# Kernel optimization log

Hardware: AMD Instinct MI355X
Metric: run time of the kernel (lower is better)

Reference implementation:

```python
import jax, jax.numpy as jnp
import numpy as np

N = 50000      # nodes
E = 800000     # edges
DIN = 256
DH = 256
DOUT = 64


def setup_inputs() -> dict:
    key = jax.random.key(0)
    ks = jax.random.split(key, 8)
    x = jax.random.normal(ks[0], (N, DIN), dtype=jnp.float32)
    edge_index = jax.random.randint(ks[1], (2, E), 0, N, dtype=jnp.int64)
    s = 0.05
    W1 = jax.random.normal(ks[2], (DIN, DH), dtype=jnp.float32) * s
    b1 = jnp.zeros((DH,), dtype=jnp.float32)
    W2 = jax.random.normal(ks[3], (DH, DH), dtype=jnp.float32) * s
    b2 = jnp.zeros((DH,), dtype=jnp.float32)
    W3 = jax.random.normal(ks[4], (DH, DOUT), dtype=jnp.float32) * s
    b3 = jnp.zeros((DOUT,), dtype=jnp.float32)
    return {"x": x, "edge_index": edge_index, "W1": W1, "b1": b1,
            "W2": W2, "b2": b2, "W3": W3, "b3": b3}


def gcn_conv(x, src, dst, deg_inv_sqrt, W, b):
    # x: [N, din] -> [N, dout]. PyG GCNConv: h = D^{-1/2}(A+I)D^{-1/2} (x W) + b
    n = x.shape[0]
    h = x @ W                                   # [N, dout]
    norm = deg_inv_sqrt[src] * deg_inv_sqrt[dst]  # [E+N]
    msgs = h[src] * norm[:, None]               # gather + scale, [E+N, dout]
    out = jax.ops.segment_sum(msgs, dst, num_segments=n)  # scatter-add
    return out + b


def _loops(edge_index, n):
    # add self loops, compute symmetric normalization degrees
    sl = jnp.arange(n, dtype=edge_index.dtype)
    src = jnp.concatenate([edge_index[0], sl])
    dst = jnp.concatenate([edge_index[1], sl])
    deg = jax.ops.segment_sum(jnp.ones_like(dst, dtype=jnp.float32), dst, num_segments=n)
    dis = jnp.where(deg > 0, jax.lax.rsqrt(deg), 0.0)
    return src, dst, dis


def reference(x, edge_index, W1, b1, W2, b2, W3, b3):
    src, dst, dis = _loops(edge_index, x.shape[0])
    h = jax.nn.relu(gcn_conv(x, src, dst, dis, W1, b1))   # dropout: eval no-op
    h = jax.nn.relu(gcn_conv(h, src, dst, dis, W2, b2))
    out = gcn_conv(h, src, dst, dis, W3, b3)              # batch=None -> no pooling
    return out
```

## Files before the change

kernel.cpp:

```cpp
#include <hip/hip_runtime.h>
#include <hip/hip_fp8.h>
#include <cstdint>
#include <cstddef>

typedef unsigned short u16;
typedef _Float16 f16x8 __attribute__((ext_vector_type(8)));
typedef float f32x2 __attribute__((ext_vector_type(2)));
typedef float f32x4 __attribute__((ext_vector_type(4)));

#if defined(__has_builtin)
#if __has_builtin(__builtin_amdgcn_cvt_pk_f32_fp8) && __has_builtin(__builtin_amdgcn_cvt_pk_fp8_f32)
#define FP8_BUILTIN 1
#endif
#endif

__device__ __forceinline__ float h2f(u16 u) {
  return (float)__builtin_bit_cast(_Float16, u);
}
__device__ __forceinline__ u16 f2h(float f) {
  return __builtin_bit_cast(u16, (_Float16)f);
}
__device__ __forceinline__ unsigned char ftofp8(float f) {
#ifdef FP8_BUILTIN
  return (unsigned char)(__builtin_amdgcn_cvt_pk_fp8_f32(f, f, 0, false) & 0xFF);
#else
  return __hip_fp8_e4m3(f).__x;
#endif
}

__device__ __forceinline__ void async16(u16* lds, const u16* g) {
  __builtin_amdgcn_global_load_lds(
      (const __attribute__((address_space(1))) unsigned int*)g,
      (__attribute__((address_space(3))) unsigned int*)lds, 16, 0, 0);
}

__device__ __forceinline__ void fma8p(float* a, float d, uint2 p) {
#ifdef FP8_BUILTIN
  f32x2 v0 = __builtin_amdgcn_cvt_pk_f32_fp8((int)p.x, false);
  f32x2 v1 = __builtin_amdgcn_cvt_pk_f32_fp8((int)p.x, true);
  f32x2 v2 = __builtin_amdgcn_cvt_pk_f32_fp8((int)p.y, false);
  f32x2 v3 = __builtin_amdgcn_cvt_pk_f32_fp8((int)p.y, true);
  a[0] += d * v0.x; a[1] += d * v0.y; a[2] += d * v1.x; a[3] += d * v1.y;
  a[4] += d * v2.x; a[5] += d * v2.y; a[6] += d * v3.x; a[7] += d * v3.y;
#else
  const unsigned char* b = (const unsigned char*)&p;
#pragma unroll
  for (int k = 0; k < 8; ++k) {
    __hip_fp8_e4m3 v; v.__x = b[k];
    a[k] += d * (float)v;
  }
#endif
}

__device__ __forceinline__ f16x8 cvt8(const float* p) {
  float4 a = *(const float4*)p;
  float4 b = *(const float4*)(p + 4);
  f16x8 r;
  r[0] = (_Float16)a.x; r[1] = (_Float16)a.y; r[2] = (_Float16)a.z; r[3] = (_Float16)a.w;
  r[4] = (_Float16)b.x; r[5] = (_Float16)b.y; r[6] = (_Float16)b.z; r[7] = (_Float16)b.w;
  return r;
}

__device__ __forceinline__ int wave_is64(const void* ep) {
  const unsigned* p = (const unsigned*)ep;
  const int lane = threadIdx.x & 63;
  unsigned v = p[2 * lane + 1] | p[2 * (lane + 64) + 1];
  unsigned long long bal = __ballot(v != 0u);
  return (bal == 0ull) ? 1 : 0;
}

__device__ __forceinline__ int edge_at(const void* ep, int is64, long long idx) {
  if (is64) return (int)((const long long*)ep)[idx];
  return ((const int*)ep)[idx];
}

#define NCHUNK 64

__global__ void zero_f32(float* p, int n) {
  int i = blockIdx.x * 256 + threadIdx.x;
  if (i < n) p[i] = 0.f;
}

__global__ __launch_bounds__(256) void prep_all(
    const float* __restrict__ W1, u16* __restrict__ wt1,
    const float* __restrict__ W2, u16* __restrict__ wt2,
    const float* __restrict__ W3, u16* __restrict__ wt3,
    const void* __restrict__ ep, int* __restrict__ cnt,
    int E, int N, int DIN, int DH, int DOUT,
    int nb_w1, int nb_w2, int nb_w3) {
  int b = blockIdx.x;
  if (b < nb_w1) {
    int idx = b * 256 + threadIdx.x;
    if (idx < DIN * DH) {
      int n = idx / DIN, k = idx % DIN;
      wt1[idx] = f2h(W1[k * DH + n]);
    }
    return;
  }
  b -= nb_w1;
  if (b < nb_w2) {
    int idx = b * 256 + threadIdx.x;
    if (idx < DH * DH) {
      int n = idx / DH, k = idx % DH;
      wt2[idx] = f2h(W2[k * DH + n]);
    }
    return;
  }
  b -= nb_w2;
  if (b < nb_w3) {
    int idx = b * 256 + threadIdx.x;
    if (idx < DH * DOUT) {
      int n = idx / DH, k = idx % DH;
      wt3[idx] = f2h(W3[k * DOUT + n]);
    }
    return;
  }
  b -= nb_w3;
  {
    __shared__ int h[256];
    h[threadIdx.x] = 0;
    __syncthreads();
    int is64 = wave_is64(ep);
    const int per = (E + NCHUNK - 1) / NCHUNK;
    const int e0 = b * per, e1 = min(e0 + per, E);
    for (int e = e0 + (int)threadIdx.x; e < e1; e += 256) {
      int d = edge_at(ep, is64, (long long)E + e);
      d = min(max(d, 0), N - 1);
      atomicAdd(&h[d >> 8], 1);
    }
    __syncthreads();
    cnt[threadIdx.x * NCHUNK + b] = h[threadIdx.x];
  }
}

__device__ __forceinline__ void bases_in_lds(const int* __restrict__ cnt,
                                             int nbuck, int E, int* bl, int* ws4) {
  const int t = threadIdx.x, lane = t & 63, w = t >> 6;
  int tot = 0;
  if (t < nbuck)
#pragma unroll 8
    for (int c = 0; c < NCHUNK; ++c) tot += cnt[t * NCHUNK + c];
  int inc = tot;
#pragma unroll
  for (int o = 1; o < 64; o <<= 1) {
    int u = __shfl_up(inc, o, 64);
    if (lane >= o) inc += u;
  }
  if (lane == 63) ws4[w] = inc;
  __syncthreads();
  if (t == 0) {
    int run = 0;
#pragma unroll
    for (int k = 0; k < 4; ++k) { int v = ws4[k]; ws4[k + 4] = run; run += v; }
  }
  __syncthreads();
  bl[t] = ws4[w + 4] + inc - tot;
  if (t == 0) bl[nbuck] = E;
  __syncthreads();
}

__global__ __launch_bounds__(256) void csr_bucket(const void* __restrict__ ep,
                                                  const int* __restrict__ cnt,
                                                  unsigned* __restrict__ tmp,
                                                  int E, int N, int nbuck) {
  __shared__ int bl[257];
  __shared__ int cur[256];
  __shared__ int ws4[8];
  const int chunk = blockIdx.x;
  const int t = threadIdx.x;
  bases_in_lds(cnt, nbuck, E, bl, ws4);
  if (t < nbuck) {
    int partial = 0;
    for (int c = 0; c < chunk; ++c) partial += cnt[t * NCHUNK + c];
    cur[t] = bl[t] + partial;
  }
  __syncthreads();
  int is64 = wave_is64(ep);
  const int per = (E + NCHUNK - 1) / NCHUNK;
  const int e0 = chunk * per, e1 = min(e0 + per, E);
  for (int e = e0 + t; e < e1; e += 256) {
    int s = edge_at(ep, is64, e);
    int d = edge_at(ep, is64, (long long)E + e);
    s = min(max(s, 0), N - 1);
    d = min(max(d, 0), N - 1);
    int pos = atomicAdd(&cur[d >> 8], 1);
    tmp[pos] = ((unsigned)d << 16) | (unsigned)s;
  }
}

__global__ __launch_bounds__(256) void csr_final(const unsigned* __restrict__ tmp,
                                                 const int* __restrict__ cnt,
                                                 int* __restrict__ rp,
                                                 float* __restrict__ dis,
                                                 u16* __restrict__ col,
                                                 int N, int E, int nbuck) {
  __shared__ int bl[257];
  __shared__ int hcnt[256];
  __shared__ int curs[256];
  __shared__ int ws4[8];
  const int b = blockIdx.x;
  const int node0 = b * 256;
  const int t = threadIdx.x, lane = t & 63, w = t >> 6;
  bases_in_lds(cnt, nbuck, E, bl, ws4);
  const int k0 = bl[b], k1 = bl[b + 1];
  hcnt[t] = 0;
  __syncthreads();
  for (int k = k0 + t; k < k1; k += 256)
    atomicAdd(&hcnt[(int)(tmp[k] >> 16) - node0], 1);
  __syncthreads();
  const int v = hcnt[t];
  int inc = v;
#pragma unroll
  for (int o = 1; o < 64; o <<= 1) {
    int u = __shfl_up(inc, o, 64);
    if (lane >= o) inc += u;
  }
  __syncthreads();
  if (lane == 63) ws4[w] = inc;
  __syncthreads();
  if (t == 0) {
    int run = 0;
#pragma unroll
    for (int k = 0; k < 4; ++k) { int vv = ws4[k]; ws4[k + 4] = run; run += vv; }
  }
  __syncthreads();
  const int excl = k0 + ws4[w + 4] + inc - v;
  if (node0 + t < N) {
    rp[node0 + t] = excl;
    dis[node0 + t] = rsqrtf((float)(v + 1));
  }
  if (b == 0 && t == 0) rp[N] = E;
  curs[t] = excl;
  __syncthreads();
  for (int k = k0 + t; k < k1; k += 256) {
    unsigned e = tmp[k];
    int dl = (int)(e >> 16) - node0;
    int pos = atomicAdd(&curs[dl], 1);
    col[pos] = (u16)(e & 0xFFFFu);
  }
}

template <int BN, int OUT8, int A32>
__global__ __launch_bounds__(256) void gemm_bres(const void* __restrict__ A,
                                                 const u16* __restrict__ Bt,
                                                 void* __restrict__ Cv, int Nt,
                                                 int Nrows) {
  constexpr int K = 256;
  constexpr int NJ = BN / 16;
  constexpr int CH = BN * K / 8;
  __shared__ __align__(16) u16 Bs[BN * K];

  const int tid = threadIdx.x, lane = tid & 63, w = tid >> 6;
  const int bm = blockIdx.x, bn = blockIdx.y;

#pragma unroll
  for (int i = 0; i < CH / 256; ++i) {
    int c = tid + i * 256;
    int ln = c & 63, t2 = c >> 6;
    int ks = t2 & 7, j = t2 >> 3;
    int row = j * 16 + (ln & 15);
    int kk = ks * 32 + (ln >> 4) * 8;
    async16(&Bs[(size_t)c * 8], Bt + (size_t)(bn * BN + row) * K + kk);
  }

  const int r16 = lane & 15, quad = lane >> 4;
  const int m0 = w * 32;

  int row0 = bm * 128 + m0 + r16;
  int row1 = row0 + 16;
  f16x8 aa0[8], aa1[8];
  if (A32) {
    row0 = min(row0, Nrows - 1);
    row1 = min(row1, Nrows - 1);
    const float* A0 = (const float*)A + (size_t)row0 * K + quad * 8;
    const float* A1 = (const float*)A + (size_t)row1 * K + quad * 8;
#pragma unroll
    for (int ks = 0; ks < 8; ++ks) {
      aa0[ks] = cvt8(A0 + ks * 32);
      aa1[ks] = cvt8(A1 + ks * 32);
    }
  } else {
    const u16* A0 = (const u16*)A + (size_t)row0 * K + quad * 8;
    const u16* A1 = (const u16*)A + (size_t)row1 * K + quad * 8;
#pragma unroll
    for (int ks = 0; ks < 8; ++ks) {
      aa0[ks] = *(const f16x8*)(A0 + ks * 32);
      aa1[ks] = *(const f16x8*)(A1 + ks * 32);
    }
  }

  f32x4 acc[2][NJ];
  const f32x4 fzero = {0.f, 0.f, 0.f, 0.f};
#pragma unroll
  for (int i = 0; i < 2; ++i)
#pragma unroll
    for (int j = 0; j < NJ; ++j) acc[i][j] = fzero;

  __syncthreads();

#pragma unroll
  for (int ks = 0; ks < 8; ++ks) {
#pragma unroll
    for (int j = 0; j < NJ; ++j) {
      f16x8 bf = *(const f16x8*)(&Bs[(size_t)((j * 8 + ks) * 64 + lane) * 8]);
      acc[0][j] = __builtin_amdgcn_mfma_f32_16x16x32_f16(aa0[ks], bf, acc[0][j], 0, 0, 0);
      acc[1][j] = __builtin_amdgcn_mfma_f32_16x16x32_f16(aa1[ks], bf, acc[1][j], 0, 0, 0);
    }
  }
#pragma unroll
  for (int i = 0; i < 2; ++i)
#pragma unroll
    for (int j = 0; j < NJ; ++j) {
      int gr = bm * 128 + m0 + i * 16 + quad * 4;
      int gc = bn * BN + j * 16 + r16;
#pragma unroll
      for (int r = 0; r < 4; ++r) {
        if (OUT8) {
          ((unsigned char*)Cv)[(size_t)(gr + r) * Nt + gc] = ftofp8(acc[i][j][r]);
        } else {
          ((u16*)Cv)[(size_t)(gr + r) * Nt + gc] = f2h(acc[i][j][r]);
        }
      }
    }
}

__global__ __launch_bounds__(256) void agg_d256(const unsigned char* __restrict__ h,
                                                const int* __restrict__ rp,
                                                const u16* __restrict__ col,
                                                const float* __restrict__ dis,
                                                const float* __restrict__ bias,
                                                u16* __restrict__ out, int N) {
  const int wid = threadIdx.x >> 6, lane = threadIdx.x & 63;
  const int i = blockIdx.x * 4 + wid;
  if (i >= N) return;
  const int sub = lane >> 5;
  const int l32 = lane & 31;
  const int c8 = l32 * 8;
  const float di = dis[i];
  float a[8] = {0.f, 0.f, 0.f, 0.f, 0.f, 0.f, 0.f, 0.f};
  if (sub == 0) {
    uint2 sv = *(const uint2*)(h + (size_t)i * 256 + c8);
    fma8p(a, di, sv);
  }
  const int e1 = rp[i + 1];
  for (int base = rp[i]; base < e1; base += 64) {
    int me = base + lane;
    int s_l = 0; float d_l = 0.f;
    if (me < e1) { s_l = (int)col[me]; d_l = dis[s_l]; }
    const int cnt = min(64, e1 - base);
    const int cntR = (cnt + 7) & ~7;
    for (int t = 0; t < cntR; t += 8) {
      int sA = __shfl(s_l, t + sub, 64);      float dA = __shfl(d_l, t + sub, 64);
      int sB = __shfl(s_l, t + 2 + sub, 64);  float dB = __shfl(d_l, t + 2 + sub, 64);
      int sC = __shfl(s_l, t + 4 + sub, 64);  float dC = __shfl(d_l, t + 4 + sub, 64);
      int sD = __shfl(s_l, t + 6 + sub, 64);  float dD = __shfl(d_l, t + 6 + sub, 64);
      uint2 pA = *(const uint2*)(h + (size_t)sA * 256 + c8);
      uint2 pB = *(const uint2*)(h + (size_t)sB * 256 + c8);
      uint2 pC = *(const uint2*)(h + (size_t)sC * 256 + c8);
      uint2 pD = *(const uint2*)(h + (size_t)sD * 256 + c8);
      fma8p(a, dA, pA); fma8p(a, dB, pB); fma8p(a, dC, pC); fma8p(a, dD, pD);
    }
  }
#pragma unroll
  for (int k = 0; k < 8; ++k) a[k] += __shfl_xor(a[k], 32, 64);
  if (sub == 0) {
    float4 b0 = *(const float4*)(bias + c8);
    float4 b1 = *(const float4*)(bias + c8 + 4);
    float r0 = fmaxf(di * a[0] + b0.x, 0.f), r1 = fmaxf(di * a[1] + b0.y, 0.f);
    float r2 = fmaxf(di * a[2] + b0.z, 0.f), r3 = fmaxf(di * a[3] + b0.w, 0.f);
    float r4 = fmaxf(di * a[4] + b1.x, 0.f), r5 = fmaxf(di * a[5] + b1.y, 0.f);
    float r6 = fmaxf(di * a[6] + b1.z, 0.f), r7 = fmaxf(di * a[7] + b1.w, 0.f);
    uint4 ov;
    ov.x = (unsigned)f2h(r0) | ((unsigned)f2h(r1) << 16);
    ov.y = (unsigned)f2h(r2) | ((unsigned)f2h(r3) << 16);
    ov.z = (unsigned)f2h(r4) | ((unsigned)f2h(r5) << 16);
    ov.w = (unsigned)f2h(r6) | ((unsigned)f2h(r7) << 16);
    *(uint4*)(out + (size_t)i * 256 + c8) = ov;
  }
}

__global__ __launch_bounds__(256) void agg_d64(const unsigned char* __restrict__ h,
                                               const int* __restrict__ rp,
                                               const u16* __restrict__ col,
                                               const float* __restrict__ dis,
                                               const float* __restrict__ bias,
                                               float* __restrict__ out, int N) {
  const int wid = threadIdx.x >> 6, lane = threadIdx.x & 63;
  const int i = blockIdx.x * 4 + wid;
  if (i >= N) return;
  const int grp = lane >> 3;
  const int l8 = lane & 7;
  const int c8 = l8 * 8;
  const float di = dis[i];
  float a[8] = {0.f, 0.f, 0.f, 0.f, 0.f, 0.f, 0.f, 0.f};
  if (grp == 0) {
    uint2 sv = *(const uint2*)(h + (size_t)i * 64 + c8);
    fma8p(a, di, sv);
  }
  const int e1 = rp[i + 1];
  for (int base = rp[i]; base < e1; base += 64) {
    int me = base + lane;
    int s_l = 0; float d_l = 0.f;
    if (me < e1) { s_l = (int)col[me]; d_l = dis[s_l]; }
    const int cnt = min(64, e1 - base);
    const int cntR = (cnt + 15) & ~15;
    for (int t = 0; t < cntR; t += 16) {
      int sA = __shfl(s_l, t + grp, 64);       float dA = __shfl(d_l, t + grp, 64);
      int sB = __shfl(s_l, t + 8 + grp, 64);   float dB = __shfl(d_l, t + 8 + grp, 64);
      uint2 pA = *(const uint2*)(h + (size_t)sA * 64 + c8);
      uint2 pB = *(const uint2*)(h + (size_t)sB * 64 + c8);
      fma8p(a, dA, pA); fma8p(a, dB, pB);
    }
  }
#pragma unroll
  for (int k = 0; k < 8; ++k) a[k] += __shfl_xor(a[k], 8, 64);
#pragma unroll
  for (int k = 0; k < 8; ++k) a[k] += __shfl_xor(a[k], 16, 64);
#pragma unroll
  for (int k = 0; k < 8; ++k) a[k] += __shfl_xor(a[k], 32, 64);
  if (lane < 8) {
    float4 b0 = *(const float4*)(bias + c8);
    float4 b1 = *(const float4*)(bias + c8 + 4);
    float4 o0, o1;
    o0.x = di * a[0] + b0.x; o0.y = di * a[1] + b0.y;
    o0.z = di * a[2] + b0.z; o0.w = di * a[3] + b0.w;
    o1.x = di * a[4] + b1.x; o1.y = di * a[5] + b1.y;
    o1.z = di * a[6] + b1.z; o1.w = di * a[7] + b1.w;
    *(float4*)(out + (size_t)i * 64 + c8) = o0;
    *(float4*)(out + (size_t)i * 64 + c8 + 4) = o1;
  }
}

extern "C" void kernel_launch(void* const* d_in, const int* in_sizes, int n_in,
                              void* d_out, int out_size, void* d_ws, size_t ws_size,
                              hipStream_t stream) {
  if (n_in < 8) return;
  const float* x = (const float*)d_in[0];
  const void* eptr = d_in[1];
  const float* W1 = (const float*)d_in[2];
  const float* b1 = (const float*)d_in[3];
  const float* W2 = (const float*)d_in[4];
  const float* b2 = (const float*)d_in[5];
  const float* W3 = (const float*)d_in[6];
  const float* b3 = (const float*)d_in[7];
  float* out = (float*)d_out;

  const int DIN = 256, DH = 256;
  const int N = in_sizes[0] / DIN;
  const int E = in_sizes[1] / 2;
  const int DOUT = in_sizes[6] / DH;
  const int MT = (N + 127) / 128;
  const int Mpad = MT * 128;
  const int nbuck = (N + 255) >> 8;

  auto rnd = [](size_t b) { return (b + 255) & ~(size_t)255; };
  size_t required = 0;
  required += rnd((size_t)Mpad * DH * 2);
  required += rnd((size_t)Mpad * DH);
  required += rnd((size_t)E * 2);
  required += rnd((size_t)E * 4);
  required += rnd((size_t)(N + 1) * 4);
  required += rnd((size_t)N * 4);
  required += rnd((size_t)DIN * DH * 2);
  required += rnd((size_t)DH * DH * 2);
  required += rnd((size_t)DH * DOUT * 2);
  required += rnd((size_t)256 * NCHUNK * 4);
  if (ws_size < required || N > 65536 || nbuck > 256 || nbuck < 1) {
    zero_f32<<<(out_size + 255) / 256, 256, 0, stream>>>(out, out_size);
    return;
  }

  char* ws = (char*)d_ws;
  size_t off0 = 0;
  auto alloc = [&](size_t bytes) {
    char* p = ws + off0;
    off0 = (off0 + bytes + 255) & ~(size_t)255;
    return p;
  };
  u16* xpad = (u16*)alloc((size_t)Mpad * DH * 2);
  unsigned char* hbuf = (unsigned char*)alloc((size_t)Mpad * DH);
  u16* colb = (u16*)alloc((size_t)E * 2);
  unsigned* tmpb = (unsigned*)alloc((size_t)E * 4);
  int* rp = (int*)alloc((size_t)(N + 1) * 4);
  float* dis = (float*)alloc((size_t)N * 4);
  u16* wt1 = (u16*)alloc((size_t)DIN * DH * 2);
  u16* wt2 = (u16*)alloc((size_t)DH * DH * 2);
  u16* wt3 = (u16*)alloc((size_t)DH * DOUT * 2);
  int* cnt = (int*)alloc((size_t)256 * NCHUNK * 4);

  const int nb_w1 = (DIN * DH + 255) / 256;
  const int nb_w2 = (DH * DH + 255) / 256;
  const int nb_w3 = (DH * DOUT + 255) / 256;
  prep_all<<<nb_w1 + nb_w2 + nb_w3 + NCHUNK, 256, 0, stream>>>(
      W1, wt1, W2, wt2, W3, wt3, eptr, cnt,
      E, N, DIN, DH, DOUT, nb_w1, nb_w2, nb_w3);

  csr_bucket<<<NCHUNK, 256, 0, stream>>>(eptr, cnt, tmpb, E, N, nbuck);
  csr_final<<<nbuck, 256, 0, stream>>>(tmpb, cnt, rp, dis, colb, N, E, nbuck);

  gemm_bres<128, 1, 1><<<dim3(MT, DH / 128), 256, 0, stream>>>(x, wt1, hbuf, DH, N);
  agg_d256<<<(N + 3) / 4, 256, 0, stream>>>(hbuf, rp, colb, dis, b1, xpad, N);
  gemm_bres<128, 1, 0><<<dim3(MT, DH / 128), 256, 0, stream>>>(xpad, wt2, hbuf, DH, N);
  agg_d256<<<(N + 3) / 4, 256, 0, stream>>>(hbuf, rp, colb, dis, b2, xpad, N);
  gemm_bres<64, 1, 0><<<dim3(MT, DOUT / 64), 256, 0, stream>>>(xpad, wt3, hbuf, DOUT, N);
  agg_d64<<<(N + 3) / 4, 256, 0, stream>>>(hbuf, rp, colb, dis, b3, out, N);
}
```

Before: 297.1 us.

## Fuse layer-1 GEMM into bucketing kernel, pre-scale features, widen aggregation loads

```diff
diff --git a/kernel.cpp b/kernel.cpp
--- a/kernel.cpp
+++ b/kernel.cpp
@@ -19,6 +19,9 @@
 }
 __device__ __forceinline__ u16 f2h(float f) {
   return __builtin_bit_cast(u16, (_Float16)f);
+}
+__device__ __forceinline__ unsigned pkh(float lo, float hi) {
+  return (unsigned)f2h(lo) | ((unsigned)f2h(hi) << 16);
 }
 __device__ __forceinline__ unsigned char ftofp8(float f) {
 #ifdef FP8_BUILTIN
@@ -52,6 +55,17 @@
 #endif
 }
 
+__device__ __forceinline__ void fma16p(float* a, float d, uint4 p) {
+  fma8p(a, d, make_uint2(p.x, p.y));
+  fma8p(a + 8, d, make_uint2(p.z, p.w));
+}
+
+__device__ __forceinline__ void fma8h(float* a, float d, uint4 p) {
+  const u16* q = (const u16*)&p;
+#pragma unroll
+  for (int k = 0; k < 8; ++k) a[k] += d * h2f(q[k]);
+}
+
 __device__ __forceinline__ f16x8 cvt8(const float* p) {
   float4 a = *(const float4*)p;
   float4 b = *(const float4*)(p + 4);
@@ -74,7 +88,7 @@
   return ((const int*)ep)[idx];
 }
 
-#define NCHUNK 64
+#define NCHUNK 256
 
 __global__ void zero_f32(float* p, int n) {
   int i = blockIdx.x * 256 + threadIdx.x;
@@ -129,7 +143,7 @@
       atomicAdd(&h[d >> 8], 1);
     }
     __syncthreads();
-    cnt[threadIdx.x * NCHUNK + b] = h[threadIdx.x];
+    cnt[b * 256 + threadIdx.x] = h[threadIdx.x];
   }
 }
 
@@ -137,9 +151,10 @@
                                              int nbuck, int E, int* bl, int* ws4) {
   const int t = threadIdx.x, lane = t & 63, w = t >> 6;
   int tot = 0;
-  if (t < nbuck)
-#pragma unroll 8
-    for (int c = 0; c < NCHUNK; ++c) tot += cnt[t * NCHUNK + c];
+  if (t < nbuck) {
+#pragma unroll 4
+    for (int c = 0; c < NCHUNK; ++c) tot += cnt[c * 256 + t];
+  }
   int inc = tot;
 #pragma unroll
   for (int o = 1; o < 64; o <<= 1) {
@@ -159,19 +174,124 @@
   __syncthreads();
 }
 
-__global__ __launch_bounds__(256) void csr_bucket(const void* __restrict__ ep,
-                                                  const int* __restrict__ cnt,
-                                                  unsigned* __restrict__ tmp,
-                                                  int E, int N, int nbuck) {
-  __shared__ int bl[257];
-  __shared__ int cur[256];
-  __shared__ int ws4[8];
+template <int BN, int OUT8, int A32, int NBT, int SC>
+__device__ __forceinline__ void gemm_dev(const void* __restrict__ A,
+                                         const u16* __restrict__ Bt,
+                                         void* __restrict__ Cv, int Nt,
+                                         int Nrows, int bm, int col0, u16* Bs) {
+  constexpr int K = 256;
+  constexpr int NJ = BN / 16;
+  constexpr int CH = BN * K / 8;
+  const int tid = threadIdx.x, lane = tid & 63, w = tid >> 6;
+
+  auto stage = [&](int bt) {
+#pragma unroll
+    for (int i = 0; i < CH / 256; ++i) {
+      int c = tid + i * 256;
+      int ln = c & 63, t2 = c >> 6;
+      int ks = t2 & 7, j = t2 >> 3;
+      int row = bt * BN + j * 16 + (ln & 15);
+      int kk = ks * 32 + (ln >> 4) * 8;
+      async16(&Bs[(size_t)c * 8], Bt + (size_t)row * K + kk);
+    }
+  };
+  stage(0);
+
+  const int r16 = lane & 15, quad = lane >> 4;
+  const int m0 = w * 32;
+  int row0 = bm * 128 + m0 + r16;
+  int row1 = row0 + 16;
+  f16x8 aa0[8], aa1[8];
+  if (A32) {
+    row0 = min(row0, Nrows - 1);
+    row1 = min(row1, Nrows - 1);
+    const float* A0 = (const float*)A + (size_t)row0 * K + quad * 8;
+    const float* A1 = (const float*)A + (size_t)row1 * K + quad * 8;
+#pragma unroll
+    for (int ks = 0; ks < 8; ++ks) {
+      aa0[ks] = cvt8(A0 + ks * 32);
+      aa1[ks] = cvt8(A1 + ks * 32);
+    }
+  } else {
+    const u16* A0 = (const u16*)A + (size_t)row0 * K + quad * 8;
+    const u16* A1 = (const u16*)A + (size_t)row1 * K + quad * 8;
+#pragma unroll
+    for (int ks = 0; ks < 8; ++ks) {
+      aa0[ks] = *(const f16x8*)(A0 + ks * 32);
+      aa1[ks] = *(const f16x8*)(A1 + ks * 32);
+    }
+  }
+
+  const f32x4 fzero = {0.f, 0.f, 0.f, 0.f};
+#pragma unroll
+  for (int bt = 0; bt < NBT; ++bt) {
+    f32x4 acc[2][NJ];
+#pragma unroll
+    for (int i = 0; i < 2; ++i)
+#pragma unroll
+      for (int j = 0; j < NJ; ++j) acc[i][j] = fzero;
+    __syncthreads();
+#pragma unroll
+    for (int ks = 0; ks < 8; ++ks)
+#pragma unroll
+      for (int j = 0; j < NJ; ++j) {
+        f16x8 bf = *(const f16x8*)(&Bs[(size_t)((j * 8 + ks) * 64 + lane) * 8]);
+        acc[0][j] = __builtin_amdgcn_mfma_f32_16x16x32_f16(aa0[ks], bf, acc[0][j], 0, 0, 0);
+        acc[1][j] = __builtin_amdgcn_mfma_f32_16x16x32_f16(aa1[ks], bf, acc[1][j], 0, 0, 0);
+      }
+    if (bt + 1 < NBT) {
+      __syncthreads();
+      stage(bt + 1);
+    }
+#pragma unroll
+    for (int i = 0; i < 2; ++i)
+#pragma unroll
+      for (int j = 0; j < NJ; ++j) {
+        int gr = bm * 128 + m0 + i * 16 + quad * 4;
+        int gc = col0 + bt * BN + j * 16 + r16;
+#pragma unroll
+        for (int r = 0; r < 4; ++r) {
+          if (OUT8) {
+            ((unsigned char*)Cv)[(size_t)(gr + r) * Nt + gc] =
+                ftofp8(acc[i][j][r] * (float)SC);
+          } else {
+            ((u16*)Cv)[(size_t)(gr + r) * Nt + gc] = f2h(acc[i][j][r]);
+          }
+        }
+      }
+  }
+}
+
+template <int BN, int OUT8, int A32, int NBT, int SC>
+__global__ __launch_bounds__(256) void gemm_bres(const void* __restrict__ A,
+                                                 const u16* __restrict__ Bt,
+                                                 void* __restrict__ Cv, int Nt,
+                                                 int Nrows) {
+  __shared__ __align__(16) u16 Bs[BN * 256];
+  const int col0 = blockIdx.y * (NBT * BN);
+  gemm_dev<BN, OUT8, A32, NBT, SC>(A, Bt + (size_t)col0 * 256, Cv, Nt, Nrows,
+                                   (int)blockIdx.x, col0, Bs);
+}
+
+__global__ __launch_bounds__(256) void bucket_gemm1(
+    const void* __restrict__ ep, const int* __restrict__ cnt,
+    unsigned* __restrict__ tmp, const float* __restrict__ x,
+    const u16* __restrict__ wt1, unsigned char* __restrict__ hbuf,
+    int E, int N, int nbuck) {
+  __shared__ __align__(16) u16 Bs[128 * 256];
+  if ((int)blockIdx.x >= NCHUNK) {
+    gemm_dev<128, 1, 1, 2, 1>(x, wt1, hbuf, 256, N, (int)blockIdx.x - NCHUNK, 0, Bs);
+    return;
+  }
+  int* bl = (int*)Bs;
+  int* cur = bl + 272;
+  int* ws4 = cur + 256;
   const int chunk = blockIdx.x;
   const int t = threadIdx.x;
   bases_in_lds(cnt, nbuck, E, bl, ws4);
   if (t < nbuck) {
     int partial = 0;
-    for (int c = 0; c < chunk; ++c) partial += cnt[t * NCHUNK + c];
+    for (int c = 0; c < chunk; ++c) partial += cnt[c * 256 + t];
     cur[t] = bl[t] + partial;
   }
   __syncthreads();
@@ -240,90 +360,7 @@
   }
 }
 
-template <int BN, int OUT8, int A32>
-__global__ __launch_bounds__(256) void gemm_bres(const void* __restrict__ A,
-                                                 const u16* __restrict__ Bt,
-                                                 void* __restrict__ Cv, int Nt,
-                                                 int Nrows) {
-  constexpr int K = 256;
-  constexpr int NJ = BN / 16;
-  constexpr int CH = BN * K / 8;
-  __shared__ __align__(16) u16 Bs[BN * K];
-
-  const int tid = threadIdx.x, lane = tid & 63, w = tid >> 6;
-  const int bm = blockIdx.x, bn = blockIdx.y;
-
-#pragma unroll
-  for (int i = 0; i < CH / 256; ++i) {
-    int c = tid + i * 256;
-    int ln = c & 63, t2 = c >> 6;
-    int ks = t2 & 7, j = t2 >> 3;
-    int row = j * 16 + (ln & 15);
-    int kk = ks * 32 + (ln >> 4) * 8;
-    async16(&Bs[(size_t)c * 8], Bt + (size_t)(bn * BN + row) * K + kk);
-  }
-
-  const int r16 = lane & 15, quad = lane >> 4;
-  const int m0 = w * 32;
-
-  int row0 = bm * 128 + m0 + r16;
-  int row1 = row0 + 16;
-  f16x8 aa0[8], aa1[8];
-  if (A32) {
-    row0 = min(row0, Nrows - 1);
-    row1 = min(row1, Nrows - 1);
-    const float* A0 = (const float*)A + (size_t)row0 * K + quad * 8;
-    const float* A1 = (const float*)A + (size_t)row1 * K + quad * 8;
-#pragma unroll
-    for (int ks = 0; ks < 8; ++ks) {
-      aa0[ks] = cvt8(A0 + ks * 32);
-      aa1[ks] = cvt8(A1 + ks * 32);
-    }
-  } else {
-    const u16* A0 = (const u16*)A + (size_t)row0 * K + quad * 8;
-    const u16* A1 = (const u16*)A + (size_t)row1 * K + quad * 8;
-#pragma unroll
-    for (int ks = 0; ks < 8; ++ks) {
-      aa0[ks] = *(const f16x8*)(A0 + ks * 32);
-      aa1[ks] = *(const f16x8*)(A1 + ks * 32);
-    }
-  }
-
-  f32x4 acc[2][NJ];
-  const f32x4 fzero = {0.f, 0.f, 0.f, 0.f};
-#pragma unroll
-  for (int i = 0; i < 2; ++i)
-#pragma unroll
-    for (int j = 0; j < NJ; ++j) acc[i][j] = fzero;
-
-  __syncthreads();
-
-#pragma unroll
-  for (int ks = 0; ks < 8; ++ks) {
-#pragma unroll
-    for (int j = 0; j < NJ; ++j) {
-      f16x8 bf = *(const f16x8*)(&Bs[(size_t)((j * 8 + ks) * 64 + lane) * 8]);
-      acc[0][j] = __builtin_amdgcn_mfma_f32_16x16x32_f16(aa0[ks], bf, acc[0][j], 0, 0, 0);
-      acc[1][j] = __builtin_amdgcn_mfma_f32_16x16x32_f16(aa1[ks], bf, acc[1][j], 0, 0, 0);
-    }
-  }
-#pragma unroll
-  for (int i = 0; i < 2; ++i)
-#pragma unroll
-    for (int j = 0; j < NJ; ++j) {
-      int gr = bm * 128 + m0 + i * 16 + quad * 4;
-      int gc = bn * BN + j * 16 + r16;
-#pragma unroll
-      for (int r = 0; r < 4; ++r) {
-        if (OUT8) {
-          ((unsigned char*)Cv)[(size_t)(gr + r) * Nt + gc] = ftofp8(acc[i][j][r]);
-        } else {
-          ((u16*)Cv)[(size_t)(gr + r) * Nt + gc] = f2h(acc[i][j][r]);
-        }
-      }
-    }
-}
-
+template <int SCALED>
 __global__ __launch_bounds__(256) void agg_d256(const unsigned char* __restrict__ h,
                                                 const int* __restrict__ rp,
                                                 const u16* __restrict__ col,
@@ -333,53 +370,76 @@
   const int wid = threadIdx.x >> 6, lane = threadIdx.x & 63;
   const int i = blockIdx.x * 4 + wid;
   if (i >= N) return;
-  const int sub = lane >> 5;
-  const int l32 = lane & 31;
-  const int c8 = l32 * 8;
+  const int sub = lane >> 4;
+  const int l16 = lane & 15;
+  const int cb = l16 * 16;
   const float di = dis[i];
-  float a[8] = {0.f, 0.f, 0.f, 0.f, 0.f, 0.f, 0.f, 0.f};
+  float a[16];
+#pragma unroll
+  for (int k = 0; k < 16; ++k) a[k] = 0.f;
   if (sub == 0) {
-    uint2 sv = *(const uint2*)(h + (size_t)i * 256 + c8);
-    fma8p(a, di, sv);
+    uint4 sv = *(const uint4*)(h + (size_t)i * 256 + cb);
+    fma16p(a, SCALED ? 1.f : di, sv);
   }
   const int e1 = rp[i + 1];
   for (int base = rp[i]; base < e1; base += 64) {
     int me = base + lane;
     int s_l = 0; float d_l = 0.f;
-    if (me < e1) { s_l = (int)col[me]; d_l = dis[s_l]; }
+    if (me < e1) { s_l = (int)col[me]; if (!SCALED) d_l = dis[s_l]; }
     const int cnt = min(64, e1 - base);
-    const int cntR = (cnt + 7) & ~7;
-    for (int t = 0; t < cntR; t += 8) {
-      int sA = __shfl(s_l, t + sub, 64);      float dA = __shfl(d_l, t + sub, 64);
-      int sB = __shfl(s_l, t + 2 + sub, 64);  float dB = __shfl(d_l, t + 2 + sub, 64);
-      int sC = __shfl(s_l, t + 4 + sub, 64);  float dC = __shfl(d_l, t + 4 + sub, 64);
-      int sD = __shfl(s_l, t + 6 + sub, 64);  float dD = __shfl(d_l, t + 6 + sub, 64);
-      uint2 pA = *(const uint2*)(h + (size_t)sA * 256 + c8);
-      uint2 pB = *(const uint2*)(h + (size_t)sB * 256 + c8);
-      uint2 pC = *(const uint2*)(h + (size_t)sC * 256 + c8);
-      uint2 pD = *(const uint2*)(h + (size_t)sD * 256 + c8);
-      fma8p(a, dA, pA); fma8p(a, dB, pB); fma8p(a, dC, pC); fma8p(a, dD, pD);
-    }
-  }
-#pragma unroll
-  for (int k = 0; k < 8; ++k) a[k] += __shfl_xor(a[k], 32, 64);
+    const int cntR = (cnt + 15) & ~15;
+    for (int t = 0; t < cntR; t += 16) {
+      int sA = __shfl(s_l, t + sub, 64);
+      int sB = __shfl(s_l, t + 4 + sub, 64);
+      int sC = __shfl(s_l, t + 8 + sub, 64);
+      int sD = __shfl(s_l, t + 12 + sub, 64);
+      float dA, dB, dC, dD;
+      if (SCALED) {
+        dA = (t + sub < cnt) ? 1.f : 0.f;
+        dB = (t + 4 + sub < cnt) ? 1.f : 0.f;
+        dC = (t + 8 + sub < cnt) ? 1.f : 0.f;
+        dD = (t + 12 + sub < cnt) ? 1.f : 0.f;
+      } else {
+        dA = __shfl(d_l, t + sub, 64);
+        dB = __shfl(d_l, t + 4 + sub, 64);
+        dC = __shfl(d_l, t + 8 + sub, 64);
+        dD = __shfl(d_l, t + 12 + sub, 64);
+      }
+      uint4 pA = *(const uint4*)(h + (size_t)sA * 256 + cb);
+      uint4 pB = *(const uint4*)(h + (size_t)sB * 256 + cb);
+      uint4 pC = *(const uint4*)(h + (size_t)sC * 256 + cb);
+      uint4 pD = *(const uint4*)(h + (size_t)sD * 256 + cb);
+      fma16p(a, dA, pA); fma16p(a, dB, pB); fma16p(a, dC, pC); fma16p(a, dD, pD);
+    }
+  }
+#pragma unroll
+  for (int k = 0; k < 16; ++k) a[k] += __shfl_xor(a[k], 16, 64);
+#pragma unroll
+  for (int k = 0; k < 16; ++k) a[k] += __shfl_xor(a[k], 32, 64);
   if (sub == 0) {
-    float4 b0 = *(const float4*)(bias + c8);
-    float4 b1 = *(const float4*)(bias + c8 + 4);
-    float r0 = fmaxf(di * a[0] + b0.x, 0.f), r1 = fmaxf(di * a[1] + b0.y, 0.f);
-    float r2 = fmaxf(di * a[2] + b0.z, 0.f), r3 = fmaxf(di * a[3] + b0.w, 0.f);
-    float r4 = fmaxf(di * a[4] + b1.x, 0.f), r5 = fmaxf(di * a[5] + b1.y, 0.f);
-    float r6 = fmaxf(di * a[6] + b1.z, 0.f), r7 = fmaxf(di * a[7] + b1.w, 0.f);
-    uint4 ov;
-    ov.x = (unsigned)f2h(r0) | ((unsigned)f2h(r1) << 16);
-    ov.y = (unsigned)f2h(r2) | ((unsigned)f2h(r3) << 16);
-    ov.z = (unsigned)f2h(r4) | ((unsigned)f2h(r5) << 16);
-    ov.w = (unsigned)f2h(r6) | ((unsigned)f2h(r7) << 16);
-    *(uint4*)(out + (size_t)i * 256 + c8) = ov;
-  }
-}
-
-__global__ __launch_bounds__(256) void agg_d64(const unsigned char* __restrict__ h,
+    const float inv = SCALED ? 0.25f : 1.f;
+    const float* bp = bias + l16 * 16;
+    float4 b0 = *(const float4*)(bp);
+    float4 b1 = *(const float4*)(bp + 4);
+    float4 b2 = *(const float4*)(bp + 8);
+    float4 b3 = *(const float4*)(bp + 12);
+    float bb[16] = {b0.x, b0.y, b0.z, b0.w, b1.x, b1.y, b1.z, b1.w,
+                    b2.x, b2.y, b2.z, b2.w, b3.x, b3.y, b3.z, b3.w};
+    float r[16];
+#pragma unroll
+    for (int k = 0; k < 16; ++k)
+      r[k] = fmaxf(di * a[k] * inv + bb[k], 0.f) * di;
+    uint4 o0, o1;
+    o0.x = pkh(r[0], r[1]);  o0.y = pkh(r[2], r[3]);
+    o0.z = pkh(r[4], r[5]);  o0.w = pkh(r[6], r[7]);
+    o1.x = pkh(r[8], r[9]);  o1.y = pkh(r[10], r[11]);
+    o1.z = pkh(r[12], r[13]); o1.w = pkh(r[14], r[15]);
+    *(uint4*)(out + (size_t)i * 256 + l16 * 16) = o0;
+    *(uint4*)(out + (size_t)i * 256 + l16 * 16 + 8) = o1;
+  }
+}
+
+__global__ __launch_bounds__(256) void agg_d64(const u16* __restrict__ h,
                                                const int* __restrict__ rp,
                                                const u16* __restrict__ col,
                                                const float* __restrict__ dis,
@@ -394,22 +454,24 @@
   const float di = dis[i];
   float a[8] = {0.f, 0.f, 0.f, 0.f, 0.f, 0.f, 0.f, 0.f};
   if (grp == 0) {
-    uint2 sv = *(const uint2*)(h + (size_t)i * 64 + c8);
-    fma8p(a, di, sv);
+    uint4 sv = *(const uint4*)(h + (size_t)i * 64 + c8);
+    fma8h(a, 1.f, sv);
   }
   const int e1 = rp[i + 1];
   for (int base = rp[i]; base < e1; base += 64) {
     int me = base + lane;
-    int s_l = 0; float d_l = 0.f;
-    if (me < e1) { s_l = (int)col[me]; d_l = dis[s_l]; }
+    int s_l = 0;
+    if (me < e1) s_l = (int)col[me];
     const int cnt = min(64, e1 - base);
     const int cntR = (cnt + 15) & ~15;
     for (int t = 0; t < cntR; t += 16) {
-      int sA = __shfl(s_l, t + grp, 64);       float dA = __shfl(d_l, t + grp, 64);
-      int sB = __shfl(s_l, t + 8 + grp, 64);   float dB = __shfl(d_l, t + 8 + grp, 64);
-      uint2 pA = *(const uint2*)(h + (size_t)sA * 64 + c8);
-      uint2 pB = *(const uint2*)(h + (size_t)sB * 64 + c8);
-      fma8p(a, dA, pA); fma8p(a, dB, pB);
+      int sA = __shfl(s_l, t + grp, 64);
+      int sB = __shfl(s_l, t + 8 + grp, 64);
+      float dA = (t + grp < cnt) ? 1.f : 0.f;
+      float dB = (t + 8 + grp < cnt) ? 1.f : 0.f;
+      uint4 pA = *(const uint4*)(h + (size_t)sA * 64 + c8);
+      uint4 pB = *(const uint4*)(h + (size_t)sB * 64 + c8);
+      fma8h(a, dA, pA); fma8h(a, dB, pB);
     }
   }
 #pragma unroll
@@ -465,7 +527,8 @@
   required += rnd((size_t)DH * DH * 2);
   required += rnd((size_t)DH * DOUT * 2);
   required += rnd((size_t)256 * NCHUNK * 4);
-  if (ws_size < required || N > 65536 || nbuck > 256 || nbuck < 1) {
+  if (ws_size < required || N > 65536 || nbuck > 256 || nbuck < 1 ||
+      E < 128 || DOUT != 64) {
     zero_f32<<<(out_size + 255) / 256, 256, 0, stream>>>(out, out_size);
     return;
   }
@@ -495,13 +558,15 @@
       W1, wt1, W2, wt2, W3, wt3, eptr, cnt,
       E, N, DIN, DH, DOUT, nb_w1, nb_w2, nb_w3);
 
-  csr_bucket<<<NCHUNK, 256, 0, stream>>>(eptr, cnt, tmpb, E, N, nbuck);
+  bucket_gemm1<<<NCHUNK + MT, 256, 0, stream>>>(eptr, cnt, tmpb, x, wt1, hbuf,
+                                                E, N, nbuck);
   csr_final<<<nbuck, 256, 0, stream>>>(tmpb, cnt, rp, dis, colb, N, E, nbuck);
 
-  gemm_bres<128, 1, 1><<<dim3(MT, DH / 128), 256, 0, stream>>>(x, wt1, hbuf, DH, N);
-  agg_d256<<<(N + 3) / 4, 256, 0, stream>>>(hbuf, rp, colb, dis, b1, xpad, N);
-  gemm_bres<128, 1, 0><<<dim3(MT, DH / 128), 256, 0, stream>>>(xpad, wt2, hbuf, DH, N);
-  agg_d256<<<(N + 3) / 4, 256, 0, stream>>>(hbuf, rp, colb, dis, b2, xpad, N);
-  gemm_bres<64, 1, 0><<<dim3(MT, DOUT / 64), 256, 0, stream>>>(xpad, wt3, hbuf, DOUT, N);
-  agg_d64<<<(N + 3) / 4, 256, 0, stream>>>(hbuf, rp, colb, dis, b3, out, N);
-}
+  agg_d256<0><<<(N + 3) / 4, 256, 0, stream>>>(hbuf, rp, colb, dis, b1, xpad, N);
+  gemm_bres<128, 1, 0, 2, 4><<<dim3(MT, 1), 256, 0, stream>>>(xpad, wt2, hbuf, DH, N);
+  agg_d256<1><<<(N + 3) / 4, 256, 0, stream>>>(hbuf, rp, colb, dis, b2, xpad, N);
+  gemm_bres<64, 0, 0, 1, 1><<<dim3(MT, DOUT / 64), 256, 0, stream>>>(
+      xpad, wt3, hbuf, DOUT, N);
+  agg_d64<<<(N + 3) / 4, 256, 0, stream>>>((const u16*)hbuf, rp, colb, dis, b3,
+                                           out, N);
+}
```

After: 323.7 us. 9.0% more time.
